# Performance work log

Measured on AMD Instinct MI355X. Metric: run time of the kernel, lower is better.

The kernel has to match this reference:

```python
import jax, jax.numpy as jnp
import numpy as np

DIM = 1024
N_HEADS = 16
HEAD_DIM = DIM // N_HEADS
SCALE = HEAD_DIM ** -0.5


def setup_inputs() -> dict:
    key = jax.random.key(0)
    ks = jax.random.split(key, 5)
    x = jax.random.normal(ks[0], (4, 2048, DIM), dtype=jnp.float32)
    s = DIM ** -0.5
    W_qkv = jax.random.normal(ks[1], (DIM, 3 * DIM), dtype=jnp.float32) * s
    b_qkv = jnp.zeros((3 * DIM,), dtype=jnp.float32)
    W_proj = jax.random.normal(ks[2], (DIM, DIM), dtype=jnp.float32) * s
    b_proj = jnp.zeros((DIM,), dtype=jnp.float32)
    return {"x": x, "W_qkv": W_qkv, "b_qkv": b_qkv, "W_proj": W_proj, "b_proj": b_proj}


def reference(x, W_qkv, b_qkv, W_proj, b_proj):
    B, S, D = x.shape
    qkv = x @ W_qkv + b_qkv                      # [B,S,3D]
    qkv = qkv.reshape(B, S, 3, N_HEADS, HEAD_DIM)
    qkv = jnp.transpose(qkv, (2, 0, 3, 1, 4))    # [3,B,H,S,hd]
    q, k, v = qkv[0], qkv[1], qkv[2]
    scores = jnp.einsum('bhqd,bhkd->bhqk', q, k) * SCALE  # [B,H,S,S]
    attn = jax.nn.softmax(scores, axis=-1)
    out = jnp.einsum('bhqk,bhkd->bhqd', attn, v)  # [B,H,S,hd]
    out = jnp.transpose(out, (0, 2, 1, 3)).reshape(B, S, D)
    return out @ W_proj + b_proj
```

## Files before the change

kernel.cpp:

```cpp
#include <hip/hip_runtime.h>

#define DIM   1024
#define SEQ   2048
#define NH    16
#define HD    64

typedef __attribute__((ext_vector_type(8))) short frag_ab;
typedef __attribute__((ext_vector_type(4))) float f32x4;

__device__ __forceinline__ ushort f32_bf16_rne(float f) {
  union { float f; unsigned int u; } v; v.f = f;
  unsigned int u = v.u + 0x7FFFu + ((v.u >> 16) & 1u);
  return (ushort)(u >> 16);
}

__device__ __forceinline__ void split_bf16(float f, ushort& h, ushort& l) {
  h = f32_bf16_rne(f);
  union { unsigned int u; float f; } hv; hv.u = ((unsigned int)h) << 16;
  l = f32_bf16_rne(f - hv.f);
}

__device__ __forceinline__ void gl2lds16(const void* g, void* l) {
  __builtin_amdgcn_global_load_lds(
      (const __attribute__((address_space(1))) unsigned int*)g,
      (__attribute__((address_space(3))) unsigned int*)l, 16, 0, 0);
}

__device__ __forceinline__ float exp2_fast(float x) {
  float r;
  asm("v_exp_f32 %0, %1" : "=v"(r) : "v"(x));
  return r;
}

__global__ __launch_bounds__(256) void cast_x(const float* __restrict__ x,
                                              ushort* __restrict__ xb) {
  int i = (blockIdx.x * 256 + threadIdx.x) * 8;
  float4 a = *(const float4*)(x + i);
  float4 b = *(const float4*)(x + i + 4);
  uint4 o;
  o.x = (unsigned int)f32_bf16_rne(a.x) | ((unsigned int)f32_bf16_rne(a.y) << 16);
  o.y = (unsigned int)f32_bf16_rne(a.z) | ((unsigned int)f32_bf16_rne(a.w) << 16);
  o.z = (unsigned int)f32_bf16_rne(b.x) | ((unsigned int)f32_bf16_rne(b.y) << 16);
  o.w = (unsigned int)f32_bf16_rne(b.z) | ((unsigned int)f32_bf16_rne(b.w) << 16);
  *(uint4*)(xb + i) = o;
}

template <bool SPLIT>
__global__ __launch_bounds__(256) void tcast(const float* __restrict__ in,
                                             int K, int N,
                                             ushort* __restrict__ outh,
                                             ushort* __restrict__ outl) {
  __shared__ __align__(16) ushort Th[64][72];
  __shared__ __align__(16) ushort Tl[64][72];
  const int kb = blockIdx.y * 64, nb = blockIdx.x * 64;
  const int t = threadIdx.x;
  const int kr = t >> 4, nc = (t & 15) * 4;
#pragma unroll
  for (int j = 0; j < 4; ++j) {
    int k = kr + j * 16;
    float4 v = *(const float4*)&in[(size_t)(kb + k) * N + nb + nc];
    float vv[4] = {v.x, v.y, v.z, v.w};
#pragma unroll
    for (int i = 0; i < 4; ++i) {
      if (SPLIT) {
        ushort h, l; split_bf16(vv[i], h, l);
        Th[nc + i][k] = h; Tl[nc + i][k] = l;
      } else {
        Th[nc + i][k] = f32_bf16_rne(vv[i]);
      }
    }
  }
  __syncthreads();
  const int n = t >> 2, kc = (t & 3) * 16;
  *(uint4*)&outh[(size_t)(nb + n) * K + kb + kc]     = *(const uint4*)&Th[n][kc];
  *(uint4*)&outh[(size_t)(nb + n) * K + kb + kc + 8] = *(const uint4*)&Th[n][kc + 8];
  if (SPLIT) {
    *(uint4*)&outl[(size_t)(nb + n) * K + kb + kc]     = *(const uint4*)&Tl[n][kc];
    *(uint4*)&outl[(size_t)(nb + n) * K + kb + kc + 8] = *(const uint4*)&Tl[n][kc + 8];
  }
}

__global__ __launch_bounds__(256) void qkv_mfma(
    const ushort* __restrict__ Xb, const ushort* __restrict__ Wqt,
    const float* __restrict__ bias,
    ushort* __restrict__ Qw, ushort* __restrict__ Kw, ushort* __restrict__ Vtw) {
  __shared__ __align__(16) ushort As[128 * 64];
  __shared__ __align__(16) ushort Bs[128 * 64];
  const int t = threadIdx.x, wave = t >> 6, lane = t & 63;
  const int ml = lane & 15, quad = lane >> 4;
  const int swz = ml & 7;
  const int lr = lane >> 3, lc = lane & 7;
  const int lin = blockIdx.x + blockIdx.y * 24;
  const int sl  = (lin & 7) * 192 + (lin >> 3);
  const int m0 = (sl / 24) * 128, n0 = (sl % 24) * 128;
  const int wm = (wave & 1) * 64, wn = (wave >> 1) * 64;

  const ushort* Ag = Xb  + (size_t)(m0 + wave * 8 + lr) * DIM + (lc ^ lr) * 8;
  const ushort* Bg = Wqt + (size_t)(n0 + wave * 8 + lr) * DIM + (lc ^ lr) * 8;

  f32x4 acc[4][4];
#pragma unroll
  for (int i = 0; i < 4; ++i)
#pragma unroll
    for (int j = 0; j < 4; ++j) acc[i][j] = (f32x4){0.f, 0.f, 0.f, 0.f};

  for (int k0 = 0; k0 < DIM; k0 += 64) {
    __syncthreads();
#pragma unroll
    for (int i = 0; i < 4; ++i) {
      gl2lds16(Ag + (size_t)(i * 32) * DIM + k0, &As[(wave * 8 + i * 32) * 64]);
      gl2lds16(Bg + (size_t)(i * 32) * DIM + k0, &Bs[(wave * 8 + i * 32) * 64]);
    }
    __syncthreads();
#pragma unroll
    for (int kk = 0; kk < 2; ++kk) {
      frag_ab af[4], bfr[4];
#pragma unroll
      for (int im = 0; im < 4; ++im)
        af[im] = *(const frag_ab*)&As[(wm + im * 16 + ml) * 64 +
                                      (((kk * 4 + quad) ^ swz) * 8)];
#pragma unroll
      for (int in_ = 0; in_ < 4; ++in_)
        bfr[in_] = *(const frag_ab*)&Bs[(wn + in_ * 16 + ml) * 64 +
                                        (((kk * 4 + quad) ^ swz) * 8)];
#pragma unroll
      for (int im = 0; im < 4; ++im)
#pragma unroll
        for (int in_ = 0; in_ < 4; ++in_)
          acc[im][in_] = __builtin_amdgcn_mfma_f32_16x16x32_bf16(
              af[im], bfr[in_], acc[im][in_], 0, 0, 0);
    }
  }

  const int t3 = n0 >> 10;
  const int b  = m0 >> 11;
  const int s0 = (m0 & (SEQ - 1)) + wm + quad * 4;
#pragma unroll
  for (int in_ = 0; in_ < 4; ++in_) {
    int n = n0 + wn + in_ * 16 + ml;
    int h = (n >> 6) & 15, d = n & 63;
    float bv = bias[n];
    size_t bh = (size_t)(b * NH + h);
    if (t3 == 2) {
#pragma unroll
      for (int im = 0; im < 4; ++im) {
        int s = s0 + im * 16;
        ushort4 v;
        v.x = f32_bf16_rne(acc[im][in_][0] + bv);
        v.y = f32_bf16_rne(acc[im][in_][1] + bv);
        v.z = f32_bf16_rne(acc[im][in_][2] + bv);
        v.w = f32_bf16_rne(acc[im][in_][3] + bv);
        *(ushort4*)&Vtw[(bh * HD + d) * SEQ + s] = v;
      }
    } else {
      ushort* dst = (t3 == 0) ? Qw : Kw;
#pragma unroll
      for (int im = 0; im < 4; ++im)
#pragma unroll
        for (int r = 0; r < 4; ++r)
          dst[(bh * SEQ + s0 + im * 16 + r) * HD + d] =
              f32_bf16_rne(acc[im][in_][r] + bv);
    }
  }
}

__global__ __launch_bounds__(512, 8) void attn_kernel(
    const ushort* Qw, const ushort* __restrict__ Kw,
    const ushort* __restrict__ Vtw, ushort* Ohw, ushort* Olw) {
  __shared__ __align__(16) ushort KsA[4096], KsB[4096];
  __shared__ __align__(16) ushort VsA[4096], VsB[4096];
  __shared__ __align__(16) ushort PsL[8][1024];

  const int t    = threadIdx.x;
  const int bid  = blockIdx.x;
  const int sbid = (bid & 7) * 128 + (bid >> 3);
  const int bh   = sbid >> 4;
  const int qt   = sbid & 15;
  const int lane = t & 63, wave = t >> 6;
  const int ml   = lane & 15, quad = lane >> 4;
  const int swz  = ml & 7;
  const int rot  = (ml >> 3) << 2;
  const int lrow = lane >> 3, lw = lane & 7;

  const size_t qbase  = ((size_t)bh * SEQ + qt * 128) * HD;
  const size_t kbase0 = (size_t)bh * SEQ * HD;
  const size_t vbase0 = (size_t)bh * HD * SEQ;

  const frag_ab a_q0 =
      *(const frag_ab*)(Qw + qbase + (size_t)(wave * 16 + ml) * HD + quad * 8);
  const frag_ab a_q1 =
      *(const frag_ab*)(Qw + qbase + (size_t)(wave * 16 + ml) * HD + 32 + quad * 8);

  const ushort* kg = Kw  + kbase0 + (size_t)(wave * 8 + lrow) * HD  + (lw ^ lrow) * 8;
  const ushort* vg = Vtw + vbase0 + (size_t)(wave * 8 + lrow) * SEQ + (lw ^ lrow) * 8;

  gl2lds16(kg, &KsA[wave * 512]);
  gl2lds16(vg, &VsA[wave * 512]);
  __syncthreads();

  f32x4 O[4];
#pragma unroll
  for (int c = 0; c < 4; ++c) O[c] = (f32x4){0.f, 0.f, 0.f, 0.f};
  float lsum = 0.f;
  const float kscale = 0.125f * 1.4426950408889634f;

#define ATTN_STEP(KT, KS_, VS_, KSN, VSN)                                      \
  {                                                                            \
    if ((KT) < 31) {                                                           \
      gl2lds16(kg + (size_t)((KT) + 1) * (64 * HD), &KSN[wave * 512]);         \
      gl2lds16(vg + (size_t)((KT) + 1) * 64,        &VSN[wave * 512]);         \
    }                                                                          \
    f32x4 sc[4];                                                               \
    __builtin_amdgcn_s_setprio(1);                                             \
    _Pragma("unroll")                                                          \
    for (int c = 0; c < 4; ++c) {                                              \
      sc[c] = (f32x4){0.f, 0.f, 0.f, 0.f};                                     \
      frag_ab bk0 = *(const frag_ab*)&KS_[(c * 16 + ml) * 64 +                 \
                                          ((quad ^ swz) * 8)];                 \
      sc[c] = __builtin_amdgcn_mfma_f32_16x16x32_bf16(bk0, a_q0, sc[c], 0, 0, 0); \
      frag_ab bk1 = *(const frag_ab*)&KS_[(c * 16 + ml) * 64 +                 \
                                          (((4 + quad) ^ swz) * 8)];           \
      sc[c] = __builtin_amdgcn_mfma_f32_16x16x32_bf16(bk1, a_q1, sc[c], 0, 0, 0); \
    }                                                                          \
    __builtin_amdgcn_s_setprio(0);                                             \
    _Pragma("unroll")                                                          \
    for (int c = 0; c < 4; ++c) {                                              \
      unsigned int uu[4];                                                      \
      _Pragma("unroll")                                                        \
      for (int r = 0; r < 4; ++r) {                                            \
        float p = exp2_fast(fmaf(sc[c][r], kscale, -12.0f));                   \
        union { float f; unsigned int u; } pv_; pv_.f = p;                     \
        unsigned int u = pv_.u & 0xffff0000u;                                  \
        union { unsigned int u; float f; } tf_; tf_.u = u;                     \
        lsum += tf_.f;                                                         \
        uu[r] = u;                                                             \
      }                                                                        \
      unsigned int w0 = (uu[0] >> 16) | (uu[1] & 0xffff0000u);                 \
      unsigned int w1 = (uu[2] >> 16) | (uu[3] & 0xffff0000u);                 \
      int wrd = (((c * 2 + (quad >> 1)) ^ swz) + rot) & 7;                     \
      char* pdst = (char*)&PsL[wave][0] + ml * 128 + wrd * 16 + (quad & 1) * 8;\
      uint2 wv; wv.x = w0; wv.y = w1;                                          \
      *(uint2*)pdst = wv;                                                      \
    }                                                                          \
    _Pragma("unroll")                                                          \
    for (int ks = 0; ks < 2; ++ks) {                                           \
      int rwd = ((((ks * 4 + quad) ^ swz) + rot) & 7);                         \
      frag_ab ap = *(const frag_ab*)((const char*)&PsL[wave][0] + ml * 128 +   \
                                     rwd * 16);                                \
      __builtin_amdgcn_s_setprio(1);                                           \
      _Pragma("unroll")                                                        \
      for (int c = 0; c < 4; ++c) {                                            \
        frag_ab bv = *(const frag_ab*)&VS_[(c * 16 + ml) * 64 +                \
                                           (((ks * 4 + quad) ^ swz) * 8)];     \
        O[c] = __builtin_amdgcn_mfma_f32_16x16x32_bf16(ap, bv, O[c], 0, 0, 0); \
      }                                                                        \
      __builtin_amdgcn_s_setprio(0);                                           \
    }                                                                          \
    __syncthreads();                                                           \
  }

  for (int kt = 0; kt < 32; kt += 2) {
    ATTN_STEP(kt,     KsA, VsA, KsB, VsB)
    ATTN_STEP(kt + 1, KsB, VsB, KsA, VsA)
  }
#undef ATTN_STEP

  lsum += __shfl_xor(lsum, 16, 64);
  lsum += __shfl_xor(lsum, 32, 64);
  float linv[4];
#pragma unroll
  for (int r = 0; r < 4; ++r)
    linv[r] = 1.0f / __shfl(lsum, quad * 4 + r, 64);

  const int q0 = qt * 128 + wave * 16 + quad * 4;
#pragma unroll
  for (int r = 0; r < 4; ++r) {
    size_t rowbase = ((size_t)bh * SEQ + q0 + r) * HD;
#pragma unroll
    for (int c = 0; c < 4; ++c) {
      float f = O[c][r] * linv[r];
      ushort h, l; split_bf16(f, h, l);
      Ohw[rowbase + c * 16 + ml] = h;
      Olw[rowbase + c * 16 + ml] = l;
    }
  }
}

__global__ __launch_bounds__(256) void proj_mfma(
    const ushort* __restrict__ Oh, const ushort* __restrict__ Ol,
    const ushort* __restrict__ Wph, const ushort* __restrict__ Wpl,
    const float* __restrict__ bias, float* __restrict__ out) {
  __shared__ __align__(16) ushort As[128 * 64];
  __shared__ __align__(16) ushort Bs[128 * 64];
  const int t = threadIdx.x, wave = t >> 6, lane = t & 63;
  const int ml = lane & 15, quad = lane >> 4;
  const int swz = ml & 7;
  const int lr = lane >> 3, lc = lane & 7;
  const int lin = blockIdx.x + blockIdx.y * 8;
  const int sl  = (lin & 7) * 64 + (lin >> 3);
  const int m0 = (sl >> 3) * 128, n0 = (sl & 7) * 128;
  const int wm = (wave & 1) * 64, wn = (wave >> 1) * 64;
  const int b = m0 >> 11, s0r = m0 & (SEQ - 1);

  f32x4 acc[4][4];
#pragma unroll
  for (int i = 0; i < 4; ++i)
#pragma unroll
    for (int j = 0; j < 4; ++j) acc[i][j] = (f32x4){0.f, 0.f, 0.f, 0.f};

  for (int kt = 0; kt < 48; ++kt) {
    int ph = kt >> 4;
    int h  = kt & 15;
    int kv = h * 64;
    const ushort* Asrc = (ph == 1) ? Ol : Oh;
    const ushort* Bsrc = (ph == 2) ? Wpl : Wph;
    const ushort* Ag = Asrc + (((size_t)(b * NH + h) * SEQ) + s0r + wave * 8 + lr)
                              * HD + (lc ^ lr) * 8;
    const ushort* Bg = Bsrc + (size_t)(n0 + wave * 8 + lr) * DIM + kv + (lc ^ lr) * 8;
    __syncthreads();
#pragma unroll
    for (int i = 0; i < 4; ++i) {
      gl2lds16(Ag + (size_t)(i * 32) * HD,  &As[(wave * 8 + i * 32) * 64]);
      gl2lds16(Bg + (size_t)(i * 32) * DIM, &Bs[(wave * 8 + i * 32) * 64]);
    }
    __syncthreads();
#pragma unroll
    for (int kk = 0; kk < 2; ++kk) {
      frag_ab af[4], bfr[4];
#pragma unroll
      for (int im = 0; im < 4; ++im)
        af[im] = *(const frag_ab*)&As[(wm + im * 16 + ml) * 64 +
                                      (((kk * 4 + quad) ^ swz) * 8)];
#pragma unroll
      for (int in_ = 0; in_ < 4; ++in_)
        bfr[in_] = *(const frag_ab*)&Bs[(wn + in_ * 16 + ml) * 64 +
                                        (((kk * 4 + quad) ^ swz) * 8)];
#pragma unroll
      for (int im = 0; im < 4; ++im)
#pragma unroll
        for (int in_ = 0; in_ < 4; ++in_)
          acc[im][in_] = __builtin_amdgcn_mfma_f32_16x16x32_bf16(
              af[im], bfr[in_], acc[im][in_], 0, 0, 0);
    }
  }

#pragma unroll
  for (int in_ = 0; in_ < 4; ++in_) {
    int n = n0 + wn + in_ * 16 + ml;
    float bv = bias[n];
#pragma unroll
    for (int im = 0; im < 4; ++im)
#pragma unroll
      for (int r = 0; r < 4; ++r) {
        int m = m0 + wm + im * 16 + quad * 4 + r;
        out[(size_t)m * DIM + n] = acc[im][in_][r] + bv;
      }
  }
}

extern "C" void kernel_launch(void* const* d_in, const int* in_sizes, int n_in,
                              void* d_out, int out_size, void* d_ws, size_t ws_size,
                              hipStream_t stream) {
  const float* x      = (const float*)d_in[0];
  const float* W_qkv  = (const float*)d_in[1];
  const float* b_qkv  = (const float*)d_in[2];
  const float* W_proj = (const float*)d_in[3];
  const float* b_proj = (const float*)d_in[4];
  float* out = (float*)d_out;

  char* ws = (char*)d_ws;
  ushort* Xb  = (ushort*)(ws);
  ushort* Wqt = (ushort*)(ws + 16777216ull);
  ushort* Qw  = (ushort*)(ws + 23068672ull);
  ushort* Kw  = (ushort*)(ws + 39845888ull);
  ushort* Vtw = (ushort*)(ws + 56623104ull);
  ushort* Wph = (ushort*)(ws + 73400320ull);
  ushort* Wpl = (ushort*)(ws + 75497472ull);
  ushort* Ohw = Xb;
  ushort* Olw = Qw;

  cast_x<<<dim3(4096), 256, 0, stream>>>(x, Xb);
  tcast<false><<<dim3(48, 16), 256, 0, stream>>>(W_qkv, DIM, 3 * DIM, Wqt, nullptr);
  tcast<true><<<dim3(16, 16), 256, 0, stream>>>(W_proj, DIM, DIM, Wph, Wpl);
  qkv_mfma<<<dim3(24, 64), 256, 0, stream>>>(Xb, Wqt, b_qkv, Qw, Kw, Vtw);
  attn_kernel<<<dim3(1024), 512, 0, stream>>>(Qw, Kw, Vtw, Ohw, Olw);
  proj_mfma<<<dim3(8, 64), 256, 0, stream>>>(Ohw, Olw, Wph, Wpl, b_proj, out);
}
```

Baseline: 306.5 us.

## Double-buffer LDS tiles in QKV and projection GEMMs; simplify P swizzle

The QKV and output-projection GEMMs now use two LDS buffers per operand. The next K-tile is prefetched with global_load_lds while the current tile feeds the MFMAs, with explicit vmcnt waits and raw barriers. This is meant to hide global-load latency that the old load-sync-compute loop exposed. It doubles LDS use per block, which may lower occupancy. The attention kernel also drops the rotation term from the P-tile swizzle, which could change LDS bank conflicts.

```diff
diff --git a/kernel.cpp b/kernel.cpp
--- a/kernel.cpp
+++ b/kernel.cpp
@@ -84,8 +84,8 @@
     const ushort* __restrict__ Xb, const ushort* __restrict__ Wqt,
     const float* __restrict__ bias,
     ushort* __restrict__ Qw, ushort* __restrict__ Kw, ushort* __restrict__ Vtw) {
-  __shared__ __align__(16) ushort As[128 * 64];
-  __shared__ __align__(16) ushort Bs[128 * 64];
+  __shared__ __align__(16) ushort As0[128 * 64], As1[128 * 64];
+  __shared__ __align__(16) ushort Bs0[128 * 64], Bs1[128 * 64];
   const int t = threadIdx.x, wave = t >> 6, lane = t & 63;
   const int ml = lane & 15, quad = lane >> 4;
   const int swz = ml & 7;
@@ -104,33 +104,52 @@
 #pragma unroll
     for (int j = 0; j < 4; ++j) acc[i][j] = (f32x4){0.f, 0.f, 0.f, 0.f};
 
-  for (int k0 = 0; k0 < DIM; k0 += 64) {
-    __syncthreads();
-#pragma unroll
-    for (int i = 0; i < 4; ++i) {
-      gl2lds16(Ag + (size_t)(i * 32) * DIM + k0, &As[(wave * 8 + i * 32) * 64]);
-      gl2lds16(Bg + (size_t)(i * 32) * DIM + k0, &Bs[(wave * 8 + i * 32) * 64]);
-    }
-    __syncthreads();
-#pragma unroll
-    for (int kk = 0; kk < 2; ++kk) {
-      frag_ab af[4], bfr[4];
-#pragma unroll
-      for (int im = 0; im < 4; ++im)
-        af[im] = *(const frag_ab*)&As[(wm + im * 16 + ml) * 64 +
-                                      (((kk * 4 + quad) ^ swz) * 8)];
-#pragma unroll
-      for (int in_ = 0; in_ < 4; ++in_)
-        bfr[in_] = *(const frag_ab*)&Bs[(wn + in_ * 16 + ml) * 64 +
-                                        (((kk * 4 + quad) ^ swz) * 8)];
-#pragma unroll
-      for (int im = 0; im < 4; ++im)
-#pragma unroll
-        for (int in_ = 0; in_ < 4; ++in_)
-          acc[im][in_] = __builtin_amdgcn_mfma_f32_16x16x32_bf16(
-              af[im], bfr[in_], acc[im][in_], 0, 0, 0);
-    }
-  }
+#define QKV_STEP(K0, AS, BS, ASN, BSN)                                         \
+  {                                                                            \
+    __builtin_amdgcn_s_barrier();                                              \
+    if ((K0) + 64 < DIM) {                                                     \
+      _Pragma("unroll")                                                        \
+      for (int i = 0; i < 4; ++i) {                                            \
+        gl2lds16(Ag + (size_t)(i * 32) * DIM + (K0) + 64,                      \
+                 &ASN[(wave * 8 + i * 32) * 64]);                              \
+        gl2lds16(Bg + (size_t)(i * 32) * DIM + (K0) + 64,                      \
+                 &BSN[(wave * 8 + i * 32) * 64]);                              \
+      }                                                                        \
+      asm volatile("s_waitcnt vmcnt(8)" ::: "memory");                         \
+    } else {                                                                   \
+      asm volatile("s_waitcnt vmcnt(0)" ::: "memory");                         \
+    }                                                                          \
+    __builtin_amdgcn_s_barrier();                                              \
+    _Pragma("unroll")                                                          \
+    for (int kk = 0; kk < 2; ++kk) {                                           \
+      frag_ab af[4], bfr[4];                                                   \
+      _Pragma("unroll")                                                        \
+      for (int im = 0; im < 4; ++im)                                           \
+        af[im] = *(const frag_ab*)&AS[(wm + im * 16 + ml) * 64 +               \
+                                      (((kk * 4 + quad) ^ swz) * 8)];          \
+      _Pragma("unroll")                                                        \
+      for (int in_ = 0; in_ < 4; ++in_)                                        \
+        bfr[in_] = *(const frag_ab*)&BS[(wn + in_ * 16 + ml) * 64 +            \
+                                        (((kk * 4 + quad) ^ swz) * 8)];        \
+      _Pragma("unroll")                                                        \
+      for (int im = 0; im < 4; ++im)                                           \
+        _Pragma("unroll")                                                      \
+        for (int in_ = 0; in_ < 4; ++in_)                                      \
+          acc[im][in_] = __builtin_amdgcn_mfma_f32_16x16x32_bf16(              \
+              af[im], bfr[in_], acc[im][in_], 0, 0, 0);                        \
+    }                                                                          \
+  }
+
+#pragma unroll
+  for (int i = 0; i < 4; ++i) {
+    gl2lds16(Ag + (size_t)(i * 32) * DIM, &As0[(wave * 8 + i * 32) * 64]);
+    gl2lds16(Bg + (size_t)(i * 32) * DIM, &Bs0[(wave * 8 + i * 32) * 64]);
+  }
+  for (int k0 = 0; k0 < DIM; k0 += 128) {
+    QKV_STEP(k0,      As0, Bs0, As1, Bs1)
+    QKV_STEP(k0 + 64, As1, Bs1, As0, Bs0)
+  }
+#undef QKV_STEP
 
   const int t3 = n0 >> 10;
   const int b  = m0 >> 11;
@@ -179,7 +198,6 @@
   const int lane = t & 63, wave = t >> 6;
   const int ml   = lane & 15, quad = lane >> 4;
   const int swz  = ml & 7;
-  const int rot  = (ml >> 3) << 2;
   const int lrow = lane >> 3, lw = lane & 7;
 
   const size_t qbase  = ((size_t)bh * SEQ + qt * 128) * HD;
@@ -237,16 +255,15 @@
       }                                                                        \
       unsigned int w0 = (uu[0] >> 16) | (uu[1] & 0xffff0000u);                 \
       unsigned int w1 = (uu[2] >> 16) | (uu[3] & 0xffff0000u);                 \
-      int wrd = (((c * 2 + (quad >> 1)) ^ swz) + rot) & 7;                     \
+      int wrd = (c * 2 + (quad >> 1)) ^ swz;                                   \
       char* pdst = (char*)&PsL[wave][0] + ml * 128 + wrd * 16 + (quad & 1) * 8;\
       uint2 wv; wv.x = w0; wv.y = w1;                                          \
       *(uint2*)pdst = wv;                                                      \
     }                                                                          \
     _Pragma("unroll")                                                          \
     for (int ks = 0; ks < 2; ++ks) {                                           \
-      int rwd = ((((ks * 4 + quad) ^ swz) + rot) & 7);                         \
       frag_ab ap = *(const frag_ab*)((const char*)&PsL[wave][0] + ml * 128 +   \
-                                     rwd * 16);                                \
+                                     (((ks * 4 + quad) ^ swz) * 16));          \
       __builtin_amdgcn_s_setprio(1);                                           \
       _Pragma("unroll")                                                        \
       for (int c = 0; c < 4; ++c) {                                            \
@@ -290,8 +307,8 @@
     const ushort* __restrict__ Oh, const ushort* __restrict__ Ol,
     const ushort* __restrict__ Wph, const ushort* __restrict__ Wpl,
     const float* __restrict__ bias, float* __restrict__ out) {
-  __shared__ __align__(16) ushort As[128 * 64];
-  __shared__ __align__(16) ushort Bs[128 * 64];
+  __shared__ __align__(16) ushort As0[128 * 64], As1[128 * 64];
+  __shared__ __align__(16) ushort Bs0[128 * 64], Bs1[128 * 64];
   const int t = threadIdx.x, wave = t >> 6, lane = t & 63;
   const int ml = lane & 15, quad = lane >> 4;
   const int swz = ml & 7;
@@ -308,41 +325,64 @@
 #pragma unroll
     for (int j = 0; j < 4; ++j) acc[i][j] = (f32x4){0.f, 0.f, 0.f, 0.f};
 
-  for (int kt = 0; kt < 48; ++kt) {
-    int ph = kt >> 4;
-    int h  = kt & 15;
-    int kv = h * 64;
-    const ushort* Asrc = (ph == 1) ? Ol : Oh;
-    const ushort* Bsrc = (ph == 2) ? Wpl : Wph;
-    const ushort* Ag = Asrc + (((size_t)(b * NH + h) * SEQ) + s0r + wave * 8 + lr)
-                              * HD + (lc ^ lr) * 8;
-    const ushort* Bg = Bsrc + (size_t)(n0 + wave * 8 + lr) * DIM + kv + (lc ^ lr) * 8;
-    __syncthreads();
+#define PROJ_SRC(KT, AGV, BGV)                                                 \
+    int ph_ = (KT) >> 4, h_ = (KT) & 15;                                       \
+    const ushort* Asrc_ = (ph_ == 1) ? Ol : Oh;                                \
+    const ushort* Bsrc_ = (ph_ == 2) ? Wpl : Wph;                              \
+    const ushort* AGV = Asrc_ + (((size_t)(b * NH + h_) * SEQ) + s0r +         \
+                                 wave * 8 + lr) * HD + (lc ^ lr) * 8;          \
+    const ushort* BGV = Bsrc_ + (size_t)(n0 + wave * 8 + lr) * DIM + h_ * 64 + \
+                                (lc ^ lr) * 8;
+
+#define PROJ_STEP(KT, AS, BS, ASN, BSN)                                        \
+  {                                                                            \
+    __builtin_amdgcn_s_barrier();                                              \
+    if ((KT) + 1 < 48) {                                                       \
+      PROJ_SRC((KT) + 1, Agn, Bgn)                                             \
+      _Pragma("unroll")                                                        \
+      for (int i = 0; i < 4; ++i) {                                            \
+        gl2lds16(Agn + (size_t)(i * 32) * HD,  &ASN[(wave * 8 + i * 32) * 64]);\
+        gl2lds16(Bgn + (size_t)(i * 32) * DIM, &BSN[(wave * 8 + i * 32) * 64]);\
+      }                                                                        \
+      asm volatile("s_waitcnt vmcnt(8)" ::: "memory");                         \
+    } else {                                                                   \
+      asm volatile("s_waitcnt vmcnt(0)" ::: "memory");                         \
+    }                                                                          \
+    __builtin_amdgcn_s_barrier();                                              \
+    _Pragma("unroll")                                                          \
+    for (int kk = 0; kk < 2; ++kk) {                                           \
+      frag_ab af[4], bfr[4];                                                   \
+      _Pragma("unroll")                                                        \
+      for (int im = 0; im < 4; ++im)                                           \
+        af[im] = *(const frag_ab*)&AS[(wm + im * 16 + ml) * 64 +               \
+                                      (((kk * 4 + quad) ^ swz) * 8)];          \
+      _Pragma("unroll")                                                        \
+      for (int in_ = 0; in_ < 4; ++in_)                                        \
+        bfr[in_] = *(const frag_ab*)&BS[(wn + in_ * 16 + ml) * 64 +            \
+                                        (((kk * 4 + quad) ^ swz) * 8)];        \
+      _Pragma("unroll")                                                        \
+      for (int im = 0; im < 4; ++im)                                           \
+        _Pragma("unroll")                                                      \
+        for (int in_ = 0; in_ < 4; ++in_)                                      \
+          acc[im][in_] = __builtin_amdgcn_mfma_f32_16x16x32_bf16(              \
+              af[im], bfr[in_], acc[im][in_], 0, 0, 0);                        \
+    }                                                                          \
+  }
+
+  {
+    PROJ_SRC(0, Ag0, Bg0)
 #pragma unroll
     for (int i = 0; i < 4; ++i) {
-      gl2lds16(Ag + (size_t)(i * 32) * HD,  &As[(wave * 8 + i * 32) * 64]);
-      gl2lds16(Bg + (size_t)(i * 32) * DIM, &Bs[(wave * 8 + i * 32) * 64]);
+      gl2lds16(Ag0 + (size_t)(i * 32) * HD,  &As0[(wave * 8 + i * 32) * 64]);
+      gl2lds16(Bg0 + (size_t)(i * 32) * DIM, &Bs0[(wave * 8 + i * 32) * 64]);
     }
-    __syncthreads();
-#pragma unroll
-    for (int kk = 0; kk < 2; ++kk) {
-      frag_ab af[4], bfr[4];
-#pragma unroll
-      for (int im = 0; im < 4; ++im)
-        af[im] = *(const frag_ab*)&As[(wm + im * 16 + ml) * 64 +
-                                      (((kk * 4 + quad) ^ swz) * 8)];
-#pragma unroll
-      for (int in_ = 0; in_ < 4; ++in_)
-        bfr[in_] = *(const frag_ab*)&Bs[(wn + in_ * 16 + ml) * 64 +
-                                        (((kk * 4 + quad) ^ swz) * 8)];
-#pragma unroll
-      for (int im = 0; im < 4; ++im)
-#pragma unroll
-        for (int in_ = 0; in_ < 4; ++in_)
-          acc[im][in_] = __builtin_amdgcn_mfma_f32_16x16x32_bf16(
-              af[im], bfr[in_], acc[im][in_], 0, 0, 0);
-    }
-  }
+  }
+  for (int kt = 0; kt < 48; kt += 2) {
+    PROJ_STEP(kt,     As0, Bs0, As1, Bs1)
+    PROJ_STEP(kt + 1, As1, Bs1, As0, Bs0)
+  }
+#undef PROJ_STEP
+#undef PROJ_SRC
 
 #pragma unroll
   for (int in_ = 0; in_ < 4; ++in_) {
```

Measured after the change: 304.7 us. About the same (-0.6%).
